# Optimization experiments

Measured on AMD Instinct MI355X. Metric: run time of the kernel, lower is better.

Reference implementation:

```python
import jax, jax.numpy as jnp
import numpy as np

N = 50000
E = 300000
D_IN = 128
H = 256
D_OUT = 256


def _glorot(key, shape):
    fan_in, fan_out = shape[0], shape[1]
    lim = float(np.sqrt(6.0 / (fan_in + fan_out)))
    return jax.random.uniform(key, shape, jnp.float32, -lim, lim)


def setup_inputs() -> dict:
    key = jax.random.key(0)
    ks = jax.random.split(key, 12)
    x = jax.random.normal(ks[0], (N, D_IN), jnp.float32)
    edge_index = jax.random.randint(ks[1], (2, E), 0, N, jnp.int64)
    return {
        "x": x,
        "edge_index": edge_index,
        "W1": _glorot(ks[2], (D_IN, H)),  "b1": jnp.zeros((H,), jnp.float32),
        "Wg1": _glorot(ks[3], (H, H)),    "bg1": jnp.zeros((H,), jnp.float32),
        "Wg2": _glorot(ks[4], (H, H)),    "bg2": jnp.zeros((H,), jnp.float32),
        "W2": _glorot(ks[5], (H, H)),     "b2": jnp.zeros((H,), jnp.float32),
        "W3": _glorot(ks[6], (H, D_OUT)), "b3": jnp.zeros((D_OUT,), jnp.float32),
    }


def _gcn_conv(h, src, dst, W, b):
    # PyG GCNConv: h' = D^-1/2 (A + I) D^-1/2 (h W) + b, deg counted at target with self-loops
    h = h @ W                                           # [N, H]
    deg = jnp.zeros((N,), h.dtype).at[dst].add(1.0) + 1.0
    dinv = jax.lax.rsqrt(deg)                           # deg^-1/2, [N]
    norm = dinv[src] * dinv[dst]                        # [E]
    msg = h[src] * norm[:, None]                        # gather + scale, [E, H]
    agg = jax.ops.segment_sum(msg, dst, num_segments=N)  # scatter-add
    agg = agg + h * (dinv * dinv)[:, None]              # self-loop contribution (norm = 1/deg)
    return agg + b


def reference(x, edge_index, W1, b1, Wg1, bg1, Wg2, bg2, W2, b2, W3, b3):
    src, dst = edge_index[0], edge_index[1]
    h = jax.nn.relu(x @ W1 + b1)
    h = jax.nn.relu(_gcn_conv(h, src, dst, Wg1, bg1))
    h = jax.nn.relu(_gcn_conv(h, src, dst, Wg2, bg2))
    h = jax.nn.relu(h @ W2 + b2)
    return jax.nn.softmax(h @ W3 + b3, axis=1)
```

## Files before the change

kernel.cpp:

```cpp
#include <hip/hip_runtime.h>
#include <math.h>

#define HDIM 256

typedef float floatx4 __attribute__((ext_vector_type(4)));
typedef __bf16 bf16x8 __attribute__((ext_vector_type(8)));
typedef unsigned short ushortx4 __attribute__((ext_vector_type(4)));

#define AS1C(p) ((const __attribute__((address_space(1))) void*)(p))
#define AS3(p)  ((__attribute__((address_space(3))) void*)(p))

__device__ inline unsigned short bf16_rn(float f) {
  unsigned u = __float_as_uint(f);
  return (unsigned short)((u + 0x7FFFu + ((u >> 16) & 1u)) >> 16);
}

__device__ inline void split_f32(float f, unsigned short& h, unsigned short& l) {
  unsigned short hb = bf16_rn(f);
  float hf = __uint_as_float(((unsigned)hb) << 16);
  h = hb;
  l = bf16_rn(f - hf);
}


__global__ __launch_bounds__(256)
void prep_w_kernel(const float* __restrict__ W, unsigned short* __restrict__ WH,
                   unsigned short* __restrict__ WL, int kshift) {
  int idx = blockIdx.x * 256 + threadIdx.x;
  int K = 1 << kshift;
  if (idx >= (K << 8)) return;
  int c = idx >> kshift;
  int k = idx & (K - 1);
  float f = W[(size_t)k * HDIM + c];
  unsigned short h, l;
  split_f32(f, h, l);
  WH[idx] = h;
  WL[idx] = l;
}


__global__ __launch_bounds__(256)
void deg_count_kernel(const int* __restrict__ ei, int* __restrict__ deg, int E) {
  int e = blockIdx.x * 256 + threadIdx.x;
  if (e < E) atomicAdd(&deg[ei[E + e]], 1);
}

__global__ __launch_bounds__(256)
void dinv_kernel(const int* __restrict__ deg, float* __restrict__ dinv, int n) {
  int i = blockIdx.x * 256 + threadIdx.x;
  if (i < n) dinv[i] = 1.0f / sqrtf((float)deg[i] + 1.0f);
}

__global__ __launch_bounds__(256)
void block_sum_kernel(const int* __restrict__ deg, int* __restrict__ bsum, int n) {
  __shared__ int sm[256];
  int t = threadIdx.x;
  int idx = blockIdx.x * 256 + t;
  sm[t] = (idx < n) ? deg[idx] : 0;
  __syncthreads();
  for (int off = 128; off > 0; off >>= 1) {
    if (t < off) sm[t] += sm[t + off];
    __syncthreads();
  }
  if (t == 0) bsum[blockIdx.x] = sm[0];
}

__global__ __launch_bounds__(256)
void scan_bsums_kernel(const int* __restrict__ bsum, int* __restrict__ boff,
                       int* __restrict__ rowptr, int nb, int n) {
  __shared__ int sm[256];
  int t = threadIdx.x;
  int v = (t < nb) ? bsum[t] : 0;
  sm[t] = v;
  __syncthreads();
  for (int off = 1; off < 256; off <<= 1) {
    int a = (t >= off) ? sm[t - off] : 0;
    __syncthreads();
    sm[t] += a;
    __syncthreads();
  }
  if (t < nb) boff[t] = sm[t] - v;
  if (t == 255) rowptr[n] = sm[255];
}

__global__ __launch_bounds__(256)
void scan_final_kernel(const int* __restrict__ deg, const int* __restrict__ boff,
                       int* __restrict__ rowptr, int* __restrict__ cursor, int n) {
  __shared__ int sm[256];
  int t = threadIdx.x;
  int idx = blockIdx.x * 256 + t;
  int v = (idx < n) ? deg[idx] : 0;
  sm[t] = v;
  __syncthreads();
  for (int off = 1; off < 256; off <<= 1) {
    int a = (t >= off) ? sm[t - off] : 0;
    __syncthreads();
    sm[t] += a;
    __syncthreads();
  }
  int excl = sm[t] - v + boff[blockIdx.x];
  if (idx < n) { rowptr[idx] = excl; cursor[idx] = excl; }
}

__global__ __launch_bounds__(256)
void fill_csr_kernel(const int* __restrict__ ei, int* __restrict__ cursor,
                     int* __restrict__ col, int E) {
  int e = blockIdx.x * 256 + threadIdx.x;
  if (e < E) {
    int s = ei[e];
    int d = ei[E + e];
    int p = atomicAdd(&cursor[d], 1);
    col[p] = s;
  }
}


template<bool BIAS, bool RELU>
__global__ __launch_bounds__(256, 3)
void mfma_gemm_kernel(const float* __restrict__ A,
                      const unsigned short* __restrict__ WH,
                      const unsigned short* __restrict__ WL,
                      const float* __restrict__ bias,
                      float* __restrict__ C, int M, int K) {
  __shared__ __align__(16) unsigned short AsH[128 * 40];
  __shared__ __align__(16) unsigned short AsL[128 * 40];
  __shared__ __align__(16) unsigned short BsH[4096];
  __shared__ __align__(16) unsigned short BsL[4096];

  const int tid = threadIdx.x;
  const int w = tid >> 6;
  const int l = tid & 63;
  const int l15 = l & 15;
  const int quad = l >> 4;
  const int wm = w & 1;
  const int wn = w >> 1;
  const int bm = blockIdx.y * 128;
  const int bn = blockIdx.x * 128;

  floatx4 acc[4][4];
#pragma unroll
  for (int i = 0; i < 4; ++i)
#pragma unroll
    for (int j = 0; j < 4; ++j) acc[i][j] = (floatx4){0.f, 0.f, 0.f, 0.f};

  for (int k0 = 0; k0 < K; k0 += 32) {
    float4 av[4];
#pragma unroll
    for (int i = 0; i < 4; ++i) {
      int chunk = i * 256 + tid;
      int row = chunk >> 3;
      int kc4 = chunk & 7;
      int grow = bm + row;
      if (grow > M - 1) grow = M - 1;
      av[i] = *(const float4*)(A + (size_t)grow * K + k0 + kc4 * 4);
    }

    __syncthreads();

#pragma unroll
    for (int j = 0; j < 2; ++j) {
      int L = j * 256 + w * 64 + l;
      int kc = L >> 7;
      int colL = L & 127;
      const unsigned short* gH = WH + (size_t)(bn + colL) * K + k0 + kc * 8;
      const unsigned short* gL = WL + (size_t)(bn + colL) * K + k0 + kc * 8;
      __builtin_amdgcn_global_load_lds(AS1C(gH), AS3(&BsH[(j * 256 + w * 64) * 8]), 16, 0, 0);
      __builtin_amdgcn_global_load_lds(AS1C(gL), AS3(&BsL[(j * 256 + w * 64) * 8]), 16, 0, 0);
    }

#pragma unroll
    for (int i = 0; i < 4; ++i) {
      int chunk = i * 256 + tid;
      int row = chunk >> 3;
      int kc4 = chunk & 7;
      unsigned short h0, h1, h2, h3, l0, l1, l2, l3;
      split_f32(av[i].x, h0, l0);
      split_f32(av[i].y, h1, l1);
      split_f32(av[i].z, h2, l2);
      split_f32(av[i].w, h3, l3);
      ushortx4 hv = {h0, h1, h2, h3};
      ushortx4 lv = {l0, l1, l2, l3};
      *(ushortx4*)&AsH[row * 40 + kc4 * 4] = hv;
      *(ushortx4*)&AsL[row * 40 + kc4 * 4] = lv;
    }

    __syncthreads();

    bf16x8 aH[4], aL[4];
#pragma unroll
    for (int fi = 0; fi < 4; ++fi) {
      int row = wm * 64 + fi * 16 + l15;
      aH[fi] = *(const bf16x8*)&AsH[row * 40 + quad * 8];
      aL[fi] = *(const bf16x8*)&AsL[row * 40 + quad * 8];
    }
#pragma unroll
    for (int fj = 0; fj < 4; ++fj) {
      int colL = wn * 64 + fj * 16 + l15;
      int cidx = quad * 128 + colL;
      bf16x8 bh = *(const bf16x8*)&BsH[cidx * 8];
      bf16x8 bl = *(const bf16x8*)&BsL[cidx * 8];
#pragma unroll
      for (int fi = 0; fi < 4; ++fi) {
        floatx4 t = acc[fi][fj];
        t = __builtin_amdgcn_mfma_f32_16x16x32_bf16(aH[fi], bl, t, 0, 0, 0);
        t = __builtin_amdgcn_mfma_f32_16x16x32_bf16(aL[fi], bh, t, 0, 0, 0);
        t = __builtin_amdgcn_mfma_f32_16x16x32_bf16(aH[fi], bh, t, 0, 0, 0);
        acc[fi][fj] = t;
      }
    }
  }

  float bcol[4];
#pragma unroll
  for (int fj = 0; fj < 4; ++fj)
    bcol[fj] = BIAS ? bias[bn + wn * 64 + fj * 16 + l15] : 0.f;

#pragma unroll
  for (int fi = 0; fi < 4; ++fi) {
    int rb = bm + wm * 64 + fi * 16 + quad * 4;
#pragma unroll
    for (int r = 0; r < 4; ++r) {
      int row = rb + r;
      if (row < M) {
        float* Cp = C + (size_t)row * HDIM + bn + wn * 64 + l15;
#pragma unroll
        for (int fj = 0; fj < 4; ++fj) {
          float v = acc[fi][fj][r] + bcol[fj];
          if (RELU) v = fmaxf(v, 0.f);
          Cp[fj * 16] = v;
        }
      }
    }
  }
}


__global__ __launch_bounds__(256)
void aggregate_kernel(const float* __restrict__ t, const float* __restrict__ dinv,
                      const int* __restrict__ rowptr, const int* __restrict__ col,
                      const float* __restrict__ bias, float* __restrict__ outp, int n) {
  int gw = (int)((blockIdx.x * 256 + threadIdx.x) >> 6);
  int lane = threadIdx.x & 63;
  if (gw >= n) return;
  float di = dinv[gw];
  const float4* ti = (const float4*)(t + (size_t)gw * HDIM);
  float4 v = ti[lane];
  float ss = di * di;
  float ax = v.x * ss, ay = v.y * ss, az = v.z * ss, aw = v.w * ss;
  int e0 = rowptr[gw], e1 = rowptr[gw + 1];
  for (int e = e0; e < e1; ++e) {
    int s = col[e];
    float wgt = dinv[s] * di;
    const float4* ts = (const float4*)(t + (size_t)s * HDIM);
    float4 u = ts[lane];
    ax = fmaf(u.x, wgt, ax);
    ay = fmaf(u.y, wgt, ay);
    az = fmaf(u.z, wgt, az);
    aw = fmaf(u.w, wgt, aw);
  }
  const float4* b4 = (const float4*)bias;
  float4 bb = b4[lane];
  float4 r;
  r.x = fmaxf(ax + bb.x, 0.f);
  r.y = fmaxf(ay + bb.y, 0.f);
  r.z = fmaxf(az + bb.z, 0.f);
  r.w = fmaxf(aw + bb.w, 0.f);
  ((float4*)(outp + (size_t)gw * HDIM))[lane] = r;
}


__global__ __launch_bounds__(256)
void softmax_kernel(const float* __restrict__ logits, float* __restrict__ outp, int n) {
  int gw = (int)((blockIdx.x * 256 + threadIdx.x) >> 6);
  int lane = threadIdx.x & 63;
  if (gw >= n) return;
  const float4* rp = (const float4*)(logits + (size_t)gw * HDIM);
  float4 v = rp[lane];
  float m = fmaxf(fmaxf(v.x, v.y), fmaxf(v.z, v.w));
#pragma unroll
  for (int off = 1; off < 64; off <<= 1) m = fmaxf(m, __shfl_xor(m, off));
  float ex = expf(v.x - m), ey = expf(v.y - m), ez = expf(v.z - m), ew = expf(v.w - m);
  float s = ex + ey + ez + ew;
#pragma unroll
  for (int off = 1; off < 64; off <<= 1) s += __shfl_xor(s, off);
  float inv = 1.0f / s;
  float4 r = make_float4(ex * inv, ey * inv, ez * inv, ew * inv);
  ((float4*)(outp + (size_t)gw * HDIM))[lane] = r;
}


extern "C" void kernel_launch(void* const* d_in, const int* in_sizes, int n_in,
                              void* d_out, int out_size, void* d_ws, size_t ws_size,
                              hipStream_t stream) {
  const float* x   = (const float*)d_in[0];
  const int*   ei  = (const int*)d_in[1];
  const float* W1  = (const float*)d_in[2];
  const float* b1  = (const float*)d_in[3];
  const float* Wg1 = (const float*)d_in[4];
  const float* bg1 = (const float*)d_in[5];
  const float* Wg2 = (const float*)d_in[6];
  const float* bg2 = (const float*)d_in[7];
  const float* W2  = (const float*)d_in[8];
  const float* b2  = (const float*)d_in[9];
  const float* W3  = (const float*)d_in[10];
  const float* b3  = (const float*)d_in[11];
  float* out = (float*)d_out;

  const int K1 = in_sizes[2] / HDIM;
  const int N  = in_sizes[0] / K1;
  const int E  = in_sizes[1] / 2;

  char* w = (char*)d_ws;
  auto alloc = [&](size_t bytes) -> char* {
    char* p = w;
    w += (bytes + 255) & ~(size_t)255;
    return p;
  };
  float* bufA   = (float*)alloc((size_t)N * HDIM * sizeof(float));
  float* dinv   = (float*)alloc((size_t)N * sizeof(float));
  int*   deg    = (int*)alloc((size_t)N * sizeof(int));
  int*   rowptr = (int*)alloc((size_t)(N + 1) * sizeof(int));
  int*   cursor = (int*)alloc((size_t)N * sizeof(int));
  int*   col    = (int*)alloc((size_t)E * sizeof(int));
  const int nb  = (N + 255) / 256;
  int*   bsum   = (int*)alloc((size_t)nb * sizeof(int));
  int*   boff   = (int*)alloc((size_t)nb * sizeof(int));
  unsigned short* W1tH  = (unsigned short*)alloc((size_t)HDIM * K1 * 2);
  unsigned short* W1tL  = (unsigned short*)alloc((size_t)HDIM * K1 * 2);
  unsigned short* Wg1tH = (unsigned short*)alloc((size_t)HDIM * HDIM * 2);
  unsigned short* Wg1tL = (unsigned short*)alloc((size_t)HDIM * HDIM * 2);
  unsigned short* Wg2tH = (unsigned short*)alloc((size_t)HDIM * HDIM * 2);
  unsigned short* Wg2tL = (unsigned short*)alloc((size_t)HDIM * HDIM * 2);
  unsigned short* W2tH  = (unsigned short*)alloc((size_t)HDIM * HDIM * 2);
  unsigned short* W2tL  = (unsigned short*)alloc((size_t)HDIM * HDIM * 2);
  unsigned short* W3tH  = (unsigned short*)alloc((size_t)HDIM * HDIM * 2);
  unsigned short* W3tL  = (unsigned short*)alloc((size_t)HDIM * HDIM * 2);

  const int ge = (E + 255) / 256;
  const int gn = (N + 255) / 256;
  const int kshift1 = (K1 == 128) ? 7 : 8;

  prep_w_kernel<<<(HDIM * K1 + 255) / 256, 256, 0, stream>>>(W1, W1tH, W1tL, kshift1);
  prep_w_kernel<<<(HDIM * HDIM + 255) / 256, 256, 0, stream>>>(Wg1, Wg1tH, Wg1tL, 8);
  prep_w_kernel<<<(HDIM * HDIM + 255) / 256, 256, 0, stream>>>(Wg2, Wg2tH, Wg2tL, 8);
  prep_w_kernel<<<(HDIM * HDIM + 255) / 256, 256, 0, stream>>>(W2, W2tH, W2tL, 8);
  prep_w_kernel<<<(HDIM * HDIM + 255) / 256, 256, 0, stream>>>(W3, W3tH, W3tL, 8);

  hipMemsetAsync(deg, 0, (size_t)N * sizeof(int), stream);
  deg_count_kernel<<<ge, 256, 0, stream>>>(ei, deg, E);
  dinv_kernel<<<gn, 256, 0, stream>>>(deg, dinv, N);
  block_sum_kernel<<<nb, 256, 0, stream>>>(deg, bsum, N);
  scan_bsums_kernel<<<1, 256, 0, stream>>>(bsum, boff, rowptr, nb, N);
  scan_final_kernel<<<nb, 256, 0, stream>>>(deg, boff, rowptr, cursor, N);
  fill_csr_kernel<<<ge, 256, 0, stream>>>(ei, cursor, col, E);

  dim3 ggrid(HDIM / 128, (N + 127) / 128);
  const int gagg = (N + 3) / 4;

  mfma_gemm_kernel<true, true><<<ggrid, 256, 0, stream>>>(x, W1tH, W1tL, b1, bufA, N, K1);
  mfma_gemm_kernel<false, false><<<ggrid, 256, 0, stream>>>(bufA, Wg1tH, Wg1tL, nullptr, out, N, HDIM);
  aggregate_kernel<<<gagg, 256, 0, stream>>>(out, dinv, rowptr, col, bg1, bufA, N);
  mfma_gemm_kernel<false, false><<<ggrid, 256, 0, stream>>>(bufA, Wg2tH, Wg2tL, nullptr, out, N, HDIM);
  aggregate_kernel<<<gagg, 256, 0, stream>>>(out, dinv, rowptr, col, bg2, bufA, N);
  mfma_gemm_kernel<true, true><<<ggrid, 256, 0, stream>>>(bufA, W2tH, W2tL, b2, out, N, HDIM);
  mfma_gemm_kernel<true, false><<<ggrid, 256, 0, stream>>>(out, W3tH, W3tL, b3, bufA, N, HDIM);
  softmax_kernel<<<gagg, 256, 0, stream>>>(bufA, out, N);
}
```

Before: 462.9 us.

## Store activations as pre-split bf16 hi/lo and widen GEMM tiles to full rows

GEMM and aggregation epilogues now write activations directly as bf16 hi/lo planes, so downstream GEMMs no longer re-split fp32 A tiles on the fly. A new GEMM kernel covers all 256 output columns per block, so each A row is read once, and it loads A and B tiles straight into LDS with swizzled global_load_lds. The aggregation loop prefetches two neighbour rows ahead to hide gather latency. Trade-offs are higher register and LDS use per block (occupancy hint drops to 2), in-place reads and writes through aliased __restrict__ pointers, and no double-buffering across k-steps.

```diff
diff --git a/kernel.cpp b/kernel.cpp
--- a/kernel.cpp
+++ b/kernel.cpp
@@ -6,6 +6,7 @@
 typedef float floatx4 __attribute__((ext_vector_type(4)));
 typedef __bf16 bf16x8 __attribute__((ext_vector_type(8)));
 typedef unsigned short ushortx4 __attribute__((ext_vector_type(4)));
+typedef unsigned short ushort_t;
 
 #define AS1C(p) ((const __attribute__((address_space(1))) void*)(p))
 #define AS3(p)  ((__attribute__((address_space(3))) void*)(p))
@@ -20,6 +21,10 @@
   float hf = __uint_as_float(((unsigned)hb) << 16);
   h = hb;
   l = bf16_rn(f - hf);
+}
+
+__device__ inline float bf2f(unsigned short b) {
+  return __uint_as_float(((unsigned)b) << 16);
 }
 
 
@@ -117,11 +122,12 @@
 
 template<bool BIAS, bool RELU>
 __global__ __launch_bounds__(256, 3)
-void mfma_gemm_kernel(const float* __restrict__ A,
+void mfma_gemm_splitA(const float* __restrict__ A,
                       const unsigned short* __restrict__ WH,
                       const unsigned short* __restrict__ WL,
                       const float* __restrict__ bias,
-                      float* __restrict__ C, int M, int K) {
+                      unsigned short* __restrict__ CH, unsigned short* __restrict__ CL,
+                      int M, int K) {
   __shared__ __align__(16) unsigned short AsH[128 * 40];
   __shared__ __align__(16) unsigned short AsL[128 * 40];
   __shared__ __align__(16) unsigned short BsH[4096];
@@ -222,12 +228,15 @@
     for (int r = 0; r < 4; ++r) {
       int row = rb + r;
       if (row < M) {
-        float* Cp = C + (size_t)row * HDIM + bn + wn * 64 + l15;
+        size_t base = (size_t)row * HDIM + bn + wn * 64 + l15;
 #pragma unroll
         for (int fj = 0; fj < 4; ++fj) {
           float v = acc[fi][fj][r] + bcol[fj];
           if (RELU) v = fmaxf(v, 0.f);
-          Cp[fj * 16] = v;
+          unsigned short h, lo;
+          split_f32(v, h, lo);
+          CH[base + fj * 16] = h;
+          CL[base + fj * 16] = lo;
         }
       }
     }
@@ -235,37 +244,179 @@
 }
 
 
-__global__ __launch_bounds__(256)
-void aggregate_kernel(const float* __restrict__ t, const float* __restrict__ dinv,
-                      const int* __restrict__ rowptr, const int* __restrict__ col,
-                      const float* __restrict__ bias, float* __restrict__ outp, int n) {
+template<bool BIAS, bool RELU, bool SPLIT_OUT>
+__global__ __launch_bounds__(256, 2)
+void mfma_gemm2(const unsigned short* __restrict__ AH, const unsigned short* __restrict__ AL,
+                const unsigned short* __restrict__ WH, const unsigned short* __restrict__ WL,
+                const float* __restrict__ bias,
+                float* __restrict__ C, unsigned short* __restrict__ CH,
+                unsigned short* __restrict__ CL, int M) {
+  __shared__ __align__(16) unsigned short AsH[128 * 32];
+  __shared__ __align__(16) unsigned short AsL[128 * 32];
+  __shared__ __align__(16) unsigned short BsH[32 * 256];
+  __shared__ __align__(16) unsigned short BsL[32 * 256];
+
+  const int tid = threadIdx.x;
+  const int w = tid >> 6;
+  const int l = tid & 63;
+  const int l15 = l & 15;
+  const int quad = l >> 4;
+  const int wm = w & 1;
+  const int wn = w >> 1;
+  const int bm = blockIdx.x * 128;
+
+  floatx4 acc[4][8];
+#pragma unroll
+  for (int i = 0; i < 4; ++i)
+#pragma unroll
+    for (int j = 0; j < 8; ++j) acc[i][j] = (floatx4){0.f, 0.f, 0.f, 0.f};
+
+  for (int k0 = 0; k0 < HDIM; k0 += 32) {
+    __syncthreads();
+
+#pragma unroll
+    for (int i = 0; i < 2; ++i) {
+      int L = i * 256 + tid;
+      int row = L >> 2;
+      int kcL = L & 3;
+      int kc = kcL ^ (row & 3) ^ ((row >> 2) & 3);
+      int grow = bm + row;
+      if (grow > M - 1) grow = M - 1;
+      const unsigned short* gH = AH + (size_t)grow * HDIM + k0 + kc * 8;
+      const unsigned short* gL = AL + (size_t)grow * HDIM + k0 + kc * 8;
+      __builtin_amdgcn_global_load_lds(AS1C(gH), AS3(&AsH[(i * 256 + w * 64) * 8]), 16, 0, 0);
+      __builtin_amdgcn_global_load_lds(AS1C(gL), AS3(&AsL[(i * 256 + w * 64) * 8]), 16, 0, 0);
+    }
+#pragma unroll
+    for (int j = 0; j < 4; ++j) {
+      int L = j * 256 + tid;
+      int kc = L >> 8;
+      int colL = L & 255;
+      const unsigned short* gH = WH + (size_t)colL * HDIM + k0 + kc * 8;
+      const unsigned short* gL = WL + (size_t)colL * HDIM + k0 + kc * 8;
+      __builtin_amdgcn_global_load_lds(AS1C(gH), AS3(&BsH[(j * 256 + w * 64) * 8]), 16, 0, 0);
+      __builtin_amdgcn_global_load_lds(AS1C(gL), AS3(&BsL[(j * 256 + w * 64) * 8]), 16, 0, 0);
+    }
+
+    __syncthreads();
+
+    bf16x8 aH[4], aL[4];
+#pragma unroll
+    for (int fi = 0; fi < 4; ++fi) {
+      int r = wm * 64 + fi * 16 + l15;
+      int sw = quad ^ (r & 3) ^ ((r >> 2) & 3);
+      aH[fi] = *(const bf16x8*)&AsH[(r * 4 + sw) * 8];
+      aL[fi] = *(const bf16x8*)&AsL[(r * 4 + sw) * 8];
+    }
+#pragma unroll
+    for (int fj = 0; fj < 8; ++fj) {
+      int colL = wn * 128 + fj * 16 + l15;
+      int cidx = quad * 256 + colL;
+      bf16x8 bh = *(const bf16x8*)&BsH[cidx * 8];
+      bf16x8 bl = *(const bf16x8*)&BsL[cidx * 8];
+#pragma unroll
+      for (int fi = 0; fi < 4; ++fi) {
+        floatx4 t = acc[fi][fj];
+        t = __builtin_amdgcn_mfma_f32_16x16x32_bf16(aH[fi], bl, t, 0, 0, 0);
+        t = __builtin_amdgcn_mfma_f32_16x16x32_bf16(aL[fi], bh, t, 0, 0, 0);
+        t = __builtin_amdgcn_mfma_f32_16x16x32_bf16(aH[fi], bh, t, 0, 0, 0);
+        acc[fi][fj] = t;
+      }
+    }
+  }
+
+  float bcol[8];
+#pragma unroll
+  for (int fj = 0; fj < 8; ++fj)
+    bcol[fj] = BIAS ? bias[wn * 128 + fj * 16 + l15] : 0.f;
+
+#pragma unroll
+  for (int fi = 0; fi < 4; ++fi) {
+    int rb = bm + wm * 64 + fi * 16 + quad * 4;
+#pragma unroll
+    for (int r = 0; r < 4; ++r) {
+      int row = rb + r;
+      if (row < M) {
+        size_t base = (size_t)row * HDIM + wn * 128 + l15;
+        if (SPLIT_OUT) {
+#pragma unroll
+          for (int fj = 0; fj < 8; ++fj) {
+            float v = acc[fi][fj][r] + bcol[fj];
+            if (RELU) v = fmaxf(v, 0.f);
+            unsigned short h, lo;
+            split_f32(v, h, lo);
+            CH[base + fj * 16] = h;
+            CL[base + fj * 16] = lo;
+          }
+        } else {
+#pragma unroll
+          for (int fj = 0; fj < 8; ++fj) {
+            float v = acc[fi][fj][r] + bcol[fj];
+            if (RELU) v = fmaxf(v, 0.f);
+            C[base + fj * 16] = v;
+          }
+        }
+      }
+    }
+  }
+}
+
+
+__global__ __launch_bounds__(256)
+void aggregate2_kernel(const float* __restrict__ t, const float* __restrict__ dinv,
+                       const int* __restrict__ rowptr, const int* __restrict__ col,
+                       const float* __restrict__ bias,
+                       unsigned short* __restrict__ OH, unsigned short* __restrict__ OL, int n) {
   int gw = (int)((blockIdx.x * 256 + threadIdx.x) >> 6);
   int lane = threadIdx.x & 63;
   if (gw >= n) return;
   float di = dinv[gw];
-  const float4* ti = (const float4*)(t + (size_t)gw * HDIM);
-  float4 v = ti[lane];
+  float4 v = ((const float4*)(t + (size_t)gw * HDIM))[lane];
   float ss = di * di;
-  float ax = v.x * ss, ay = v.y * ss, az = v.z * ss, aw = v.w * ss;
+  float a0 = v.x * ss, a1 = v.y * ss, a2 = v.z * ss, a3 = v.w * ss;
   int e0 = rowptr[gw], e1 = rowptr[gw + 1];
-  for (int e = e0; e < e1; ++e) {
-    int s = col[e];
-    float wgt = dinv[s] * di;
-    const float4* ts = (const float4*)(t + (size_t)s * HDIM);
-    float4 u = ts[lane];
-    ax = fmaf(u.x, wgt, ax);
-    ay = fmaf(u.y, wgt, ay);
-    az = fmaf(u.z, wgt, az);
-    aw = fmaf(u.w, wgt, aw);
-  }
-  const float4* b4 = (const float4*)bias;
-  float4 bb = b4[lane];
-  float4 r;
-  r.x = fmaxf(ax + bb.x, 0.f);
-  r.y = fmaxf(ay + bb.y, 0.f);
-  r.z = fmaxf(az + bb.z, 0.f);
-  r.w = fmaxf(aw + bb.w, 0.f);
-  ((float4*)(outp + (size_t)gw * HDIM))[lane] = r;
+  int cnt = e1 - e0;
+
+  float4 cur = make_float4(0.f, 0.f, 0.f, 0.f), nxt = cur;
+  float cw = 0.f, nw = 0.f;
+  if (cnt > 0) {
+    int s = col[e0];
+    cw = dinv[s] * di;
+    cur = ((const float4*)(t + (size_t)s * HDIM))[lane];
+  }
+  if (cnt > 1) {
+    int s = col[e0 + 1];
+    nw = dinv[s] * di;
+    nxt = ((const float4*)(t + (size_t)s * HDIM))[lane];
+  }
+  for (int i = 0; i < cnt; ++i) {
+    float4 c = cur;
+    float wgt = cw;
+    cur = nxt;
+    cw = nw;
+    if (i + 2 < cnt) {
+      int s = col[e0 + i + 2];
+      nw = dinv[s] * di;
+      nxt = ((const float4*)(t + (size_t)s * HDIM))[lane];
+    }
+    a0 = fmaf(c.x, wgt, a0);
+    a1 = fmaf(c.y, wgt, a1);
+    a2 = fmaf(c.z, wgt, a2);
+    a3 = fmaf(c.w, wgt, a3);
+  }
+
+  float4 bb = ((const float4*)bias)[lane];
+  float r0 = fmaxf(a0 + bb.x, 0.f);
+  float r1 = fmaxf(a1 + bb.y, 0.f);
+  float r2 = fmaxf(a2 + bb.z, 0.f);
+  float r3 = fmaxf(a3 + bb.w, 0.f);
+  unsigned short h0, h1, h2, h3, l0, l1, l2, l3;
+  split_f32(r0, h0, l0);
+  split_f32(r1, h1, l1);
+  split_f32(r2, h2, l2);
+  split_f32(r3, h3, l3);
+  ((ushortx4*)(OH + (size_t)gw * HDIM))[lane] = (ushortx4){h0, h1, h2, h3};
+  ((ushortx4*)(OL + (size_t)gw * HDIM))[lane] = (ushortx4){l0, l1, l2, l3};
 }
 
 
@@ -274,8 +425,7 @@
   int gw = (int)((blockIdx.x * 256 + threadIdx.x) >> 6);
   int lane = threadIdx.x & 63;
   if (gw >= n) return;
-  const float4* rp = (const float4*)(logits + (size_t)gw * HDIM);
-  float4 v = rp[lane];
+  float4 v = ((const float4*)(logits + (size_t)gw * HDIM))[lane];
   float m = fmaxf(fmaxf(v.x, v.y), fmaxf(v.z, v.w));
 #pragma unroll
   for (int off = 1; off < 64; off <<= 1) m = fmaxf(m, __shfl_xor(m, off));
@@ -284,8 +434,7 @@
 #pragma unroll
   for (int off = 1; off < 64; off <<= 1) s += __shfl_xor(s, off);
   float inv = 1.0f / s;
-  float4 r = make_float4(ex * inv, ey * inv, ez * inv, ew * inv);
-  ((float4*)(outp + (size_t)gw * HDIM))[lane] = r;
+  ((float4*)(outp + (size_t)gw * HDIM))[lane] = make_float4(ex * inv, ey * inv, ez * inv, ew * inv);
 }
 
 
@@ -316,7 +465,8 @@
     w += (bytes + 255) & ~(size_t)255;
     return p;
   };
-  float* bufA   = (float*)alloc((size_t)N * HDIM * sizeof(float));
+  unsigned short* PH = (unsigned short*)alloc((size_t)N * HDIM * 2);
+  unsigned short* PL = (unsigned short*)alloc((size_t)N * HDIM * 2);
   float* dinv   = (float*)alloc((size_t)N * sizeof(float));
   int*   deg    = (int*)alloc((size_t)N * sizeof(int));
   int*   rowptr = (int*)alloc((size_t)(N + 1) * sizeof(int));
@@ -354,15 +504,16 @@
   scan_final_kernel<<<nb, 256, 0, stream>>>(deg, boff, rowptr, cursor, N);
   fill_csr_kernel<<<ge, 256, 0, stream>>>(ei, cursor, col, E);
 
-  dim3 ggrid(HDIM / 128, (N + 127) / 128);
+  dim3 g1grid(HDIM / 128, (N + 127) / 128);
+  const int g2grid = (N + 127) / 128;
   const int gagg = (N + 3) / 4;
 
-  mfma_gemm_kernel<true, true><<<ggrid, 256, 0, stream>>>(x, W1tH, W1tL, b1, bufA, N, K1);
-  mfma_gemm_kernel<false, false><<<ggrid, 256, 0, stream>>>(bufA, Wg1tH, Wg1tL, nullptr, out, N, HDIM);
-  aggregate_kernel<<<gagg, 256, 0, stream>>>(out, dinv, rowptr, col, bg1, bufA, N);
-  mfma_gemm_kernel<false, false><<<ggrid, 256, 0, stream>>>(bufA, Wg2tH, Wg2tL, nullptr, out, N, HDIM);
-  aggregate_kernel<<<gagg, 256, 0, stream>>>(out, dinv, rowptr, col, bg2, bufA, N);
-  mfma_gemm_kernel<true, true><<<ggrid, 256, 0, stream>>>(bufA, W2tH, W2tL, b2, out, N, HDIM);
-  mfma_gemm_kernel<true, false><<<ggrid, 256, 0, stream>>>(out, W3tH, W3tL, b3, bufA, N, HDIM);
-  softmax_kernel<<<gagg, 256, 0, stream>>>(bufA, out, N);
-}
+  mfma_gemm_splitA<true, true><<<g1grid, 256, 0, stream>>>(x, W1tH, W1tL, b1, PH, PL, N, K1);
+  mfma_gemm2<false, false, false><<<g2grid, 256, 0, stream>>>(PH, PL, Wg1tH, Wg1tL, nullptr, out, nullptr, nullptr, N);
+  aggregate2_kernel<<<gagg, 256, 0, stream>>>(out, dinv, rowptr, col, bg1, PH, PL, N);
+  mfma_gemm2<false, false, false><<<g2grid, 256, 0, stream>>>(PH, PL, Wg2tH, Wg2tL, nullptr, out, nullptr, nullptr, N);
+  aggregate2_kernel<<<gagg, 256, 0, stream>>>(out, dinv, rowptr, col, bg2, PH, PL, N);
+  mfma_gemm2<true, true, true><<<g2grid, 256, 0, stream>>>(PH, PL, W2tH, W2tL, b2, nullptr, PH, PL, N);
+  mfma_gemm2<true, false, false><<<g2grid, 256, 0, stream>>>(PH, PL, W3tH, W3tL, b3, out, nullptr, nullptr, N);
+  softmax_kernel<<<gagg, 256, 0, stream>>>(out, out, N);
+}
```

Measured after the change: 481.5 us. 1.04x slower.
